# Performance work log

Hardware: AMD Instinct MI355X
Metric: run time of the kernel (lower is better)

Reference implementation:

```python
import jax, jax.numpy as jnp
import numpy as np


def setup_inputs() -> dict:
    key = jax.random.key(0)
    ks = jax.random.split(key, 6)
    Bsz, Ch, N, L = 16, 1024, 16, 4096
    return {
        "input": jax.random.normal(ks[0], (Bsz, Ch, L), jnp.float32),
        "A": jax.random.normal(ks[1], (Ch, N, 2), jnp.float32),
        "B": jax.random.normal(ks[2], (Ch, N), jnp.float32),  # unused in 'dws' mode
        "C": jax.random.normal(ks[3], (Ch, N), jnp.float32),  # unused in 'dws' mode
        "log_dt": jax.random.normal(ks[4], (Ch, N), jnp.float32) * 0.5 - 4.0,
        "E": jax.random.normal(ks[5], (Ch, N), jnp.float32),
    }


def reference(input, A, B, C, log_dt, E):
    """Kernelizer forward, mode='dws', run_mode='training'.

    discretize (simplified ZOH):
      A_real = -softplus(A[...,0]); A_imag = A[...,1]; dt = exp(log_dt)
      E_hat = E * dt; dtA = dt * (A_real + i*A_imag)        # (Ch, N)
    kernel: k[c, l] = Re( sum_n E_hat[c,n] * exp(dtA[c,n] * l) )
    output: causal depthwise conv of input with k via 2L-padded FFT.
    """
    L = input.shape[-1]
    A_real = -jax.nn.softplus(A[..., 0])                     # (Ch, N)
    A_imag = A[..., 1]                                       # (Ch, N)
    dt = jnp.exp(log_dt)                                     # (Ch, N)
    E_hat = E * dt                                           # (Ch, N)
    dtA_real = dt * A_real
    dtA_imag = dt * A_imag

    l = jnp.arange(L, dtype=input.dtype)                     # (L,)
    # real part of the complex vandermonde, fused: exp(ar*l) * cos(ai*l)
    vand = jnp.exp(dtA_real[:, :, None] * l) * jnp.cos(dtA_imag[:, :, None] * l)  # (Ch, N, L)
    k = jnp.einsum('cn,cnl->cl', E_hat, vand)                # (Ch, L)

    n_fft = 2 * L  # zero-pad so circular conv == linear causal conv
    Uf = jnp.fft.rfft(input, n=n_fft)                        # (B, Ch, L+1)
    Kf = jnp.fft.rfft(k, n=n_fft)                            # (Ch, L+1)
    y = jnp.fft.irfft(Uf * Kf, n=n_fft)[..., :L]             # (B, Ch, L)
    return y.astype(input.dtype)
```

## Files before the change

### kernel.cpp

```cpp
#include <hip/hip_runtime.h>
#include <hip/hip_bf16.h>

#define CH   1024
#define BSZ  16
#define LSEQ 4096
#define NST  16

typedef __attribute__((ext_vector_type(8))) short short8;
typedef __attribute__((ext_vector_type(4))) float f32x4;

__device__ __forceinline__ unsigned int pk2(float a, float b) {
    unsigned int ua = __float_as_uint(a);
    unsigned int ub = __float_as_uint(b);
    ua = (ua + 0x7fffu + ((ua >> 16) & 1u)) >> 16;
    ub = (ub + 0x7fffu + ((ub >> 16) & 1u)) & 0xffff0000u;
    return ua | ub;
}
__device__ __forceinline__ unsigned int pkrn(float a, float b) {
    __hip_bfloat162 h = __float22bfloat162_rn(make_float2(a, b));
    unsigned int u;
    __builtin_memcpy(&u, &h, 4);
    return u;
}
__device__ __forceinline__ float rfl(float x) {
    return __int_as_float(__builtin_amdgcn_readfirstlane(__float_as_int(x)));
}
#define DSHR(x, d) __int_as_float(__builtin_amdgcn_update_dpp(0, __float_as_int(x), 0x110 + (d), 0xf, 0xf, true))
#define DBC(x, ctrl, rm) __int_as_float(__builtin_amdgcn_update_dpp(0, __float_as_int(x), (ctrl), (rm), 0xf, true))

#define P_BYTES 12582912
#define W_BYTES 4194304

__global__ __launch_bounds__(64) void setup_k(const float* __restrict__ A,
                                              const float* __restrict__ log_dt,
                                              const float* __restrict__ E,
                                              unsigned int* __restrict__ Pw,
                                              unsigned int* __restrict__ Ww,
                                              float* __restrict__ qw) {
    __shared__ float powr[NST][65], powi[NST][65], eh[NST], klds[64];
    const int t = threadIdx.x, c = blockIdx.x;
    const int n = t & 15;
    const int idx = c * NST + n;
    float a0 = A[2 * idx], a1 = A[2 * idx + 1];
    float sp = (a0 > 20.f) ? a0 : log1pf(expf(a0));
    float dt = expf(log_dt[idx]);
    float dar = -dt * sp, dai = dt * a1;
    float ehv = E[idx] * dt;
    if (t < NST) eh[t] = ehv;
    for (int l = t >> 4; l < 65; l += 4) {
        float mg = expf(dar * (float)l);
        float s, cs;
        sincosf(dai * (float)l, &s, &cs);
        powr[n][l] = mg * cs;
        powi[n][l] = mg * s;
    }
    __syncthreads();
    float kl = 0.f;
#pragma unroll
    for (int nn = 0; nn < NST; ++nn) kl += eh[nn] * powr[nn][t];
    klds[t] = kl;
    __syncthreads();
    unsigned int* Pc = Pw + c * 3072;
    for (int kk = 0; kk < 48; ++kk) {
        int d = kk * 64 + t;
        int i = d / 48;
        int k0 = (d - i * 48) * 2;
        float vv[2];
#pragma unroll
        for (int u = 0; u < 2; ++u) {
            int k = k0 + u;
            if (k < 64) vv[u] = (k <= i) ? klds[i - k] : 0.f;
            else {
                int p = k - 64;
                int nn = p >> 1;
                vv[u] = (p & 1) ? (-eh[nn] * powi[nn][i + 1]) : (eh[nn] * powr[nn][i + 1]);
            }
        }
        Pc[d] = pk2(vv[0], vv[1]);
    }
    unsigned int* Wc = Ww + c * 1024;
    for (int kk = 0; kk < 16; ++kk) {
        int d = kk * 64 + t;
        int p = d >> 5;
        int j0 = (d & 31) * 2;
        int nn = p >> 1;
        float v0 = (p & 1) ? powi[nn][63 - j0] : powr[nn][63 - j0];
        float v1 = (p & 1) ? powi[nn][62 - j0] : powr[nn][62 - j0];
        Wc[d] = pk2(v0, v1);
    }
    if (t < 32) qw[c * 32 + t] = (t & 1) ? powi[t >> 1][64] : powr[t >> 1][64];
}

#define XT0_OFF 0
#define XT1_OFF 8192
#define S_OFF   16384
#define SIN_OFF 24704
#define SMEM_SZ 28800

__global__ __launch_bounds__(256, 4) void conv_k(const float* __restrict__ x,
                                                 const char* __restrict__ Pb,
                                                 const char* __restrict__ Wb,
                                                 const float* __restrict__ qw,
                                                 float* __restrict__ y) {
    __shared__ __align__(16) char smem[SMEM_SZ];
    const int tid  = threadIdx.x;
    const int w    = tid >> 6, lane = tid & 63;
    const int g    = lane >> 4, l15 = lane & 15;
    const int c    = blockIdx.x;

    const char* Pc = Pb + (size_t)c * 12288;
    const char* Wc = Wb + (size_t)c * 4096;
    short8 wa[2], pa[3];
    {
        int p = 16 * (w >> 1) + l15;
#pragma unroll
        for (int kt = 0; kt < 2; ++kt)
            wa[kt] = *(const short8*)(Wc + p * 128 + kt * 64 + g * 16);
        int i = 16 * w + l15;
#pragma unroll
        for (int kt = 0; kt < 3; ++kt)
            pa[kt] = *(const short8*)(Pc + i * 192 + kt * 64 + g * 16);
    }

    float q1r[4], q1i[4], q2r[4], q2i[4], q4r[4], q4i[4], q8r[4], q8i[4];
    float fr[4], fi[4], hr[4], hi[4];
#pragma unroll
    for (int k = 0; k < 4; ++k) {
        int nn = 4 * w + k;
        float ar = qw[c * 32 + 2 * nn], ai = qw[c * 32 + 2 * nn + 1];
        float b2r = fmaf(ar, ar, -(ai * ai)), b2i = 2.f * ar * ai;
        float b4r = fmaf(b2r, b2r, -(b2i * b2i)), b4i = 2.f * b2r * b2i;
        float b8r = fmaf(b4r, b4r, -(b4i * b4i)), b8i = 2.f * b4r * b4i;
        float b16r = fmaf(b8r, b8r, -(b8i * b8i)), b16i = 2.f * b8r * b8i;
        q1r[k] = rfl(ar);  q1i[k] = rfl(ai);
        q2r[k] = rfl(b2r); q2i[k] = rfl(b2i);
        q4r[k] = rfl(b4r); q4i[k] = rfl(b4i);
        q8r[k] = rfl(b8r); q8i[k] = rfl(b8i);
        float cr = ar, ci = ai;
        {
            float tr = fmaf(cr, ar, -(ci * ai)), ti = fmaf(cr, ai, ci * ar);
            cr = (l15 & 1) ? tr : cr; ci = (l15 & 1) ? ti : ci;
        }
        {
            float tr = fmaf(cr, b2r, -(ci * b2i)), ti = fmaf(cr, b2i, ci * b2r);
            cr = (l15 & 2) ? tr : cr; ci = (l15 & 2) ? ti : ci;
        }
        {
            float tr = fmaf(cr, b4r, -(ci * b4i)), ti = fmaf(cr, b4i, ci * b4r);
            cr = (l15 & 4) ? tr : cr; ci = (l15 & 4) ? ti : ci;
        }
        {
            float tr = fmaf(cr, b8r, -(ci * b8i)), ti = fmaf(cr, b8i, ci * b8r);
            cr = (l15 & 8) ? tr : cr; ci = (l15 & 8) ? ti : ci;
        }
        fr[k] = cr; fi[k] = ci;
        float tr = fmaf(cr, b16r, -(ci * b16i)), ti = fmaf(cr, b16i, ci * b16r);
        bool r3 = (lane >= 48);
        hr[k] = r3 ? tr : cr; hi[k] = r3 ? ti : ci;
    }

    int xfo[4][2], sino[4], stb[2];
#pragma unroll
    for (int nt = 0; nt < 4; ++nt) {
#pragma unroll
        for (int kt = 0; kt < 2; ++kt)
            xfo[nt][kt] = ((l15 * 128 + kt * 64 + g * 16) ^ ((l15 & 7) << 4)) + nt * 2048;
        sino[nt] = ((l15 * 64 + g * 16) ^ ((l15 & 3) << 4)) + nt * 1024;
    }
#pragma unroll
    for (int it = 0; it < 2; ++it) {
        int slot = it * 256 + tid;
        int m = slot >> 3, js = slot & 7;
        stb[it] = (m * 128 + js * 16) ^ ((m & 7) << 4);
    }
    const int ntb  = (w & 1) << 1;
    const int swb  = ((16 * (w >> 1) + 4 * g) * 65 + l15 + 16 * ntb) * 4;
    const int srb  = (8 * w * 65 + lane) * 4;
    const int sinw = (lane * 64 + 16 * w) ^ ((lane & 3) << 4);

    float* Sf = (float*)(smem + S_OFF);
    (void)Sf;

    short8 xf[4][2];
    auto rdfrags = [&](int xoff) {
#pragma unroll
        for (int nt = 0; nt < 4; ++nt)
#pragma unroll
            for (int kt = 0; kt < 2; ++kt)
                xf[nt][kt] = *(const short8*)(smem + xoff + xfo[nt][kt]);
    };

    auto gemm1 = [&]() {
        f32x4 a0 = {0.f, 0.f, 0.f, 0.f}, a1 = {0.f, 0.f, 0.f, 0.f};
        if ((w & 1) == 0) {
#pragma unroll
            for (int kt = 0; kt < 2; ++kt) {
                a0 = __builtin_amdgcn_mfma_f32_16x16x32_bf16(wa[kt], xf[0][kt], a0, 0, 0, 0);
                a1 = __builtin_amdgcn_mfma_f32_16x16x32_bf16(wa[kt], xf[1][kt], a1, 0, 0, 0);
            }
        } else {
#pragma unroll
            for (int kt = 0; kt < 2; ++kt) {
                a0 = __builtin_amdgcn_mfma_f32_16x16x32_bf16(wa[kt], xf[2][kt], a0, 0, 0, 0);
                a1 = __builtin_amdgcn_mfma_f32_16x16x32_bf16(wa[kt], xf[3][kt], a1, 0, 0, 0);
            }
        }
#pragma unroll
        for (int r = 0; r < 4; ++r) {
            *(float*)(smem + S_OFF + swb + r * 260)      = a0[r];
            *(float*)(smem + S_OFF + swb + r * 260 + 64) = a1[r];
        }
    };

    auto scan = [&]() {
        float sr[4], si[4];
#pragma unroll
        for (int k = 0; k < 4; ++k) {
            sr[k] = *(const float*)(smem + S_OFF + srb + k * 520);
            si[k] = *(const float*)(smem + S_OFF + srb + k * 520 + 260);
        }
#pragma unroll
        for (int k = 0; k < 4; ++k) {
            { float ur = DSHR(sr[k], 1), ui = DSHR(si[k], 1);
              sr[k] = fmaf(q1r[k], ur, fmaf(-q1i[k], ui, sr[k]));
              si[k] = fmaf(q1r[k], ui, fmaf(q1i[k], ur, si[k])); }
            { float ur = DSHR(sr[k], 2), ui = DSHR(si[k], 2);
              sr[k] = fmaf(q2r[k], ur, fmaf(-q2i[k], ui, sr[k]));
              si[k] = fmaf(q2r[k], ui, fmaf(q2i[k], ur, si[k])); }
            { float ur = DSHR(sr[k], 4), ui = DSHR(si[k], 4);
              sr[k] = fmaf(q4r[k], ur, fmaf(-q4i[k], ui, sr[k]));
              si[k] = fmaf(q4r[k], ui, fmaf(q4i[k], ur, si[k])); }
            { float ur = DSHR(sr[k], 8), ui = DSHR(si[k], 8);
              sr[k] = fmaf(q8r[k], ur, fmaf(-q8i[k], ui, sr[k]));
              si[k] = fmaf(q8r[k], ui, fmaf(q8i[k], ur, si[k])); }
            { float ur = DBC(sr[k], 0x142, 0xa), ui = DBC(si[k], 0x142, 0xa);
              sr[k] = fmaf(fr[k], ur, fmaf(-fi[k], ui, sr[k]));
              si[k] = fmaf(fr[k], ui, fmaf(fi[k], ur, si[k])); }
            { float ur = DBC(sr[k], 0x143, 0xc), ui = DBC(si[k], 0x143, 0xc);
              sr[k] = fmaf(hr[k], ur, fmaf(-hi[k], ui, sr[k]));
              si[k] = fmaf(hr[k], ui, fmaf(hi[k], ur, si[k])); }
        }
        unsigned int dw[4];
#pragma unroll
        for (int k = 0; k < 4; ++k) {
            float ar = __shfl_up(sr[k], 1);
            float ai = __shfl_up(si[k], 1);
            ar = (lane > 0) ? ar : 0.f;
            ai = (lane > 0) ? ai : 0.f;
            dw[k] = pkrn(ar, ai);
        }
        *(uint4*)(smem + SIN_OFF + sinw) = make_uint4(dw[0], dw[1], dw[2], dw[3]);
    };

    auto gemm2 = [&](float* yr) {
        f32x4 acc[4] = {{0.f,0.f,0.f,0.f},{0.f,0.f,0.f,0.f},{0.f,0.f,0.f,0.f},{0.f,0.f,0.f,0.f}};
#pragma unroll
        for (int nt = 0; nt < 4; ++nt) {
            acc[nt] = __builtin_amdgcn_mfma_f32_16x16x32_bf16(pa[0], xf[nt][0], acc[nt], 0, 0, 0);
            short8 sf = *(const short8*)(smem + SIN_OFF + sino[nt]);
            acc[nt] = __builtin_amdgcn_mfma_f32_16x16x32_bf16(pa[2], sf, acc[nt], 0, 0, 0);
        }
        if (w >= 2) {
#pragma unroll
            for (int nt = 0; nt < 4; ++nt)
                acc[nt] = __builtin_amdgcn_mfma_f32_16x16x32_bf16(pa[1], xf[nt][1], acc[nt], 0, 0, 0);
        }
#pragma unroll
        for (int nt = 0; nt < 4; ++nt) {
            int m = l15 + 16 * nt;
            float4 v = make_float4(acc[nt][0], acc[nt][1], acc[nt][2], acc[nt][3]);
            *(float4*)(yr + m * 64 + 16 * w + 4 * g) = v;
        }
    };

    float4 pend[4];
    const float* xr = x + (size_t)c * LSEQ;
    float*       yb = y + (size_t)c * LSEQ;
    const size_t cstride = (size_t)CH * LSEQ;

    auto ldraw = [&](const float* xp) {
#pragma unroll
        for (int it = 0; it < 2; ++it) {
            int slot = it * 256 + tid;
            pend[2 * it]     = *(const float4*)(xp + slot * 8);
            pend[2 * it + 1] = *(const float4*)(xp + slot * 8 + 4);
        }
    };
    auto stage = [&](int xoff) {
#pragma unroll
        for (int it = 0; it < 2; ++it) {
            uint4 pk;
            pk.x = pkrn(pend[2 * it].x,     pend[2 * it].y);
            pk.y = pkrn(pend[2 * it].z,     pend[2 * it].w);
            pk.z = pkrn(pend[2 * it + 1].x, pend[2 * it + 1].y);
            pk.w = pkrn(pend[2 * it + 1].z, pend[2 * it + 1].w);
            *(uint4*)(smem + xoff + stb[it]) = pk;
        }
    };

    ldraw(xr);
    stage(XT0_OFF);
    ldraw(xr + cstride);
    __syncthreads();

#pragma unroll 1
    for (int bb = 0; bb < 8; ++bb) {
        rdfrags(XT0_OFF);
        gemm1();
        __syncthreads();
        scan();
        stage(XT1_OFF);
        if (bb < 7) ldraw(xr + (size_t)(2 * bb + 2) * cstride);
        __syncthreads();
        gemm2(yb + (size_t)(2 * bb) * cstride);

        rdfrags(XT1_OFF);
        gemm1();
        __syncthreads();
        scan();
        if (bb < 7) {
            stage(XT0_OFF);
            ldraw(xr + (size_t)(2 * bb + 3) * cstride);
        }
        __syncthreads();
        gemm2(yb + (size_t)(2 * bb + 1) * cstride);
    }
}

extern "C" void kernel_launch(void* const* d_in, const int* in_sizes, int n_in,
                              void* d_out, int out_size, void* d_ws, size_t ws_size,
                              hipStream_t stream) {
    const float* x      = (const float*)d_in[0];
    const float* A      = (const float*)d_in[1];
    const float* log_dt = (const float*)d_in[4];
    const float* E      = (const float*)d_in[5];
    float* out = (float*)d_out;
    char*  ws  = (char*)d_ws;

    unsigned int* Pw = (unsigned int*)ws;
    unsigned int* Ww = (unsigned int*)(ws + P_BYTES);
    float*        qw = (float*)(ws + P_BYTES + W_BYTES);

    setup_k<<<CH, 64, 0, stream>>>(A, log_dt, E, Pw, Ww, qw);
    conv_k<<<CH, 256, 0, stream>>>(x, (const char*)Pw, (const char*)Ww, qw, out);
}
```

Baseline: 127.1 us.

## Fuse kernel setup into conv kernel and split batch across two blocks

Removes the separate setup kernel: each conv block now computes the per-channel SSM powers, kernel taps and bf16 MFMA operand fragments in shared memory itself, so the workspace round-trip and the second launch go away. The grid doubles to two blocks per channel, each handling half the batch, which raises parallelism but makes both blocks of a channel repeat the setup work. Barriers are replaced by a lighter s_waitcnt lgkmcnt(0) plus s_barrier, which no longer waits for outstanding global loads.

```diff
diff --git a/kernel.cpp b/kernel.cpp
--- a/kernel.cpp
+++ b/kernel.cpp
@@ -9,13 +9,6 @@
 typedef __attribute__((ext_vector_type(8))) short short8;
 typedef __attribute__((ext_vector_type(4))) float f32x4;
 
-__device__ __forceinline__ unsigned int pk2(float a, float b) {
-    unsigned int ua = __float_as_uint(a);
-    unsigned int ub = __float_as_uint(b);
-    ua = (ua + 0x7fffu + ((ua >> 16) & 1u)) >> 16;
-    ub = (ub + 0x7fffu + ((ub >> 16) & 1u)) & 0xffff0000u;
-    return ua | ub;
-}
 __device__ __forceinline__ unsigned int pkrn(float a, float b) {
     __hip_bfloat162 h = __float22bfloat162_rn(make_float2(a, b));
     unsigned int u;
@@ -28,98 +21,130 @@
 #define DSHR(x, d) __int_as_float(__builtin_amdgcn_update_dpp(0, __float_as_int(x), 0x110 + (d), 0xf, 0xf, true))
 #define DBC(x, ctrl, rm) __int_as_float(__builtin_amdgcn_update_dpp(0, __float_as_int(x), (ctrl), (rm), 0xf, true))
 
-#define P_BYTES 12582912
-#define W_BYTES 4194304
-
-__global__ __launch_bounds__(64) void setup_k(const float* __restrict__ A,
-                                              const float* __restrict__ log_dt,
-                                              const float* __restrict__ E,
-                                              unsigned int* __restrict__ Pw,
-                                              unsigned int* __restrict__ Ww,
-                                              float* __restrict__ qw) {
-    __shared__ float powr[NST][65], powi[NST][65], eh[NST], klds[64];
-    const int t = threadIdx.x, c = blockIdx.x;
-    const int n = t & 15;
-    const int idx = c * NST + n;
-    float a0 = A[2 * idx], a1 = A[2 * idx + 1];
-    float sp = (a0 > 20.f) ? a0 : log1pf(expf(a0));
-    float dt = expf(log_dt[idx]);
-    float dar = -dt * sp, dai = dt * a1;
-    float ehv = E[idx] * dt;
-    if (t < NST) eh[t] = ehv;
-    for (int l = t >> 4; l < 65; l += 4) {
-        float mg = expf(dar * (float)l);
-        float s, cs;
-        sincosf(dai * (float)l, &s, &cs);
-        powr[n][l] = mg * cs;
-        powi[n][l] = mg * s;
-    }
-    __syncthreads();
-    float kl = 0.f;
-#pragma unroll
-    for (int nn = 0; nn < NST; ++nn) kl += eh[nn] * powr[nn][t];
-    klds[t] = kl;
-    __syncthreads();
-    unsigned int* Pc = Pw + c * 3072;
-    for (int kk = 0; kk < 48; ++kk) {
-        int d = kk * 64 + t;
-        int i = d / 48;
-        int k0 = (d - i * 48) * 2;
-        float vv[2];
-#pragma unroll
-        for (int u = 0; u < 2; ++u) {
-            int k = k0 + u;
-            if (k < 64) vv[u] = (k <= i) ? klds[i - k] : 0.f;
-            else {
-                int p = k - 64;
-                int nn = p >> 1;
-                vv[u] = (p & 1) ? (-eh[nn] * powi[nn][i + 1]) : (eh[nn] * powr[nn][i + 1]);
-            }
-        }
-        Pc[d] = pk2(vv[0], vv[1]);
-    }
-    unsigned int* Wc = Ww + c * 1024;
-    for (int kk = 0; kk < 16; ++kk) {
-        int d = kk * 64 + t;
-        int p = d >> 5;
-        int j0 = (d & 31) * 2;
-        int nn = p >> 1;
-        float v0 = (p & 1) ? powi[nn][63 - j0] : powr[nn][63 - j0];
-        float v1 = (p & 1) ? powi[nn][62 - j0] : powr[nn][62 - j0];
-        Wc[d] = pk2(v0, v1);
-    }
-    if (t < 32) qw[c * 32 + t] = (t & 1) ? powi[t >> 1][64] : powr[t >> 1][64];
-}
-
 #define XT0_OFF 0
 #define XT1_OFF 8192
 #define S_OFF   16384
 #define SIN_OFF 24704
 #define SMEM_SZ 28800
 
+__device__ __forceinline__ void barrier_fast() {
+    asm volatile("s_waitcnt lgkmcnt(0)\n\ts_barrier" ::: "memory");
+}
+
 __global__ __launch_bounds__(256, 4) void conv_k(const float* __restrict__ x,
-                                                 const char* __restrict__ Pb,
-                                                 const char* __restrict__ Wb,
-                                                 const float* __restrict__ qw,
+                                                 const float* __restrict__ A,
+                                                 const float* __restrict__ log_dt,
+                                                 const float* __restrict__ E,
                                                  float* __restrict__ y) {
     __shared__ __align__(16) char smem[SMEM_SZ];
     const int tid  = threadIdx.x;
     const int w    = tid >> 6, lane = tid & 63;
     const int g    = lane >> 4, l15 = lane & 15;
-    const int c    = blockIdx.x;
-
-    const char* Pc = Pb + (size_t)c * 12288;
-    const char* Wc = Wb + (size_t)c * 4096;
+    const int bid  = blockIdx.x;
+    const int c    = bid >> 1;
+    const int half = bid & 1;
+
+    const size_t cstride = (size_t)CH * LSEQ;
+    const float* xr = x + ((size_t)(8 * half) * CH + c) * (size_t)LSEQ;
+    float*       yb = y + ((size_t)(8 * half) * CH + c) * (size_t)LSEQ;
+
+    int stb[2];
+#pragma unroll
+    for (int it = 0; it < 2; ++it) {
+        int slot = it * 256 + tid;
+        int m = slot >> 3, js = slot & 7;
+        stb[it] = (m * 128 + js * 16) ^ ((m & 7) << 4);
+    }
+    float4 pend[4];
+    auto ldraw = [&](const float* xp) {
+#pragma unroll
+        for (int it = 0; it < 2; ++it) {
+            int slot = it * 256 + tid;
+            pend[2 * it]     = *(const float4*)(xp + slot * 8);
+            pend[2 * it + 1] = *(const float4*)(xp + slot * 8 + 4);
+        }
+    };
+    auto stage = [&](int xoff) {
+#pragma unroll
+        for (int it = 0; it < 2; ++it) {
+            uint4 pk;
+            pk.x = pkrn(pend[2 * it].x,     pend[2 * it].y);
+            pk.y = pkrn(pend[2 * it].z,     pend[2 * it].w);
+            pk.z = pkrn(pend[2 * it + 1].x, pend[2 * it + 1].y);
+            pk.w = pkrn(pend[2 * it + 1].z, pend[2 * it + 1].w);
+            *(uint4*)(smem + xoff + stb[it]) = pk;
+        }
+    };
+
+    ldraw(xr);
+
+    float* PR = (float*)(smem + S_OFF);
+    float* PI = PR + NST * 65;
+    float* EH = (float*)(smem + SIN_OFF);
+    float* KL = EH + NST;
+    {
+        int n = tid & 15;
+        int idx0 = c * NST + n;
+        float a0 = A[2 * idx0], a1 = A[2 * idx0 + 1];
+        float sp = (a0 > 20.f) ? a0 : log1pf(expf(a0));
+        float dtv = expf(log_dt[idx0]);
+        float dar = -dtv * sp, dai = dtv * a1;
+        if (tid < NST) EH[tid] = E[idx0] * dtv;
+        for (int l = tid >> 4; l < 65; l += 16) {
+            float mg = expf(dar * (float)l);
+            float s, cs;
+            sincosf(dai * (float)l, &s, &cs);
+            PR[n * 65 + l] = mg * cs;
+            PI[n * 65 + l] = mg * s;
+        }
+    }
+    __syncthreads();
+    if (tid < 64) {
+        float kl = 0.f;
+#pragma unroll
+        for (int nn = 0; nn < NST; ++nn) kl += EH[nn] * PR[nn * 65 + tid];
+        KL[tid] = kl;
+    }
+    __syncthreads();
+
     short8 wa[2], pa[3];
     {
         int p = 16 * (w >> 1) + l15;
-#pragma unroll
-        for (int kt = 0; kt < 2; ++kt)
-            wa[kt] = *(const short8*)(Wc + p * 128 + kt * 64 + g * 16);
+        const float* tb = ((p & 1) ? PI : PR) + (p >> 1) * 65;
+#pragma unroll
+        for (int kt = 0; kt < 2; ++kt) {
+            union { short8 v; unsigned int d[4]; } u;
+#pragma unroll
+            for (int e2 = 0; e2 < 4; ++e2) {
+                int j = kt * 32 + 8 * g + 2 * e2;
+                u.d[e2] = pkrn(tb[63 - j], tb[62 - j]);
+            }
+            wa[kt] = u.v;
+        }
         int i = 16 * w + l15;
 #pragma unroll
-        for (int kt = 0; kt < 3; ++kt)
-            pa[kt] = *(const short8*)(Pc + i * 192 + kt * 64 + g * 16);
+        for (int kt = 0; kt < 2; ++kt) {
+            union { short8 v; unsigned int d[4]; } u;
+#pragma unroll
+            for (int e2 = 0; e2 < 4; ++e2) {
+                int k0 = kt * 32 + 8 * g + 2 * e2;
+                float v0 = (k0 <= i)     ? KL[i - k0]     : 0.f;
+                float v1 = (k0 + 1 <= i) ? KL[i - k0 - 1] : 0.f;
+                u.d[e2] = pkrn(v0, v1);
+            }
+            pa[kt] = u.v;
+        }
+        {
+            union { short8 v; unsigned int d[4]; } u;
+#pragma unroll
+            for (int e2 = 0; e2 < 4; ++e2) {
+                int n3 = 4 * g + e2;
+                float re = EH[n3] * PR[n3 * 65 + i + 1];
+                float im = -EH[n3] * PI[n3 * 65 + i + 1];
+                u.d[e2] = pkrn(re, im);
+            }
+            pa[2] = u.v;
+        }
     }
 
     float q1r[4], q1i[4], q2r[4], q2i[4], q4r[4], q4i[4], q8r[4], q8i[4];
@@ -127,7 +152,7 @@
 #pragma unroll
     for (int k = 0; k < 4; ++k) {
         int nn = 4 * w + k;
-        float ar = qw[c * 32 + 2 * nn], ai = qw[c * 32 + 2 * nn + 1];
+        float ar = PR[nn * 65 + 64], ai = PI[nn * 65 + 64];
         float b2r = fmaf(ar, ar, -(ai * ai)), b2i = 2.f * ar * ai;
         float b4r = fmaf(b2r, b2r, -(b2i * b2i)), b4i = 2.f * b2r * b2i;
         float b8r = fmaf(b4r, b4r, -(b4i * b4i)), b8i = 2.f * b4r * b4i;
@@ -159,27 +184,18 @@
         hr[k] = r3 ? tr : cr; hi[k] = r3 ? ti : ci;
     }
 
-    int xfo[4][2], sino[4], stb[2];
+    int xfo[4][2], sino[4];
 #pragma unroll
     for (int nt = 0; nt < 4; ++nt) {
 #pragma unroll
         for (int kt = 0; kt < 2; ++kt)
             xfo[nt][kt] = ((l15 * 128 + kt * 64 + g * 16) ^ ((l15 & 7) << 4)) + nt * 2048;
         sino[nt] = ((l15 * 64 + g * 16) ^ ((l15 & 3) << 4)) + nt * 1024;
-    }
-#pragma unroll
-    for (int it = 0; it < 2; ++it) {
-        int slot = it * 256 + tid;
-        int m = slot >> 3, js = slot & 7;
-        stb[it] = (m * 128 + js * 16) ^ ((m & 7) << 4);
     }
     const int ntb  = (w & 1) << 1;
     const int swb  = ((16 * (w >> 1) + 4 * g) * 65 + l15 + 16 * ntb) * 4;
     const int srb  = (8 * w * 65 + lane) * 4;
     const int sinw = (lane * 64 + 16 * w) ^ ((lane & 3) << 4);
-
-    float* Sf = (float*)(smem + S_OFF);
-    (void)Sf;
 
     short8 xf[4][2];
     auto rdfrags = [&](int xoff) {
@@ -273,56 +289,30 @@
         }
     };
 
-    float4 pend[4];
-    const float* xr = x + (size_t)c * LSEQ;
-    float*       yb = y + (size_t)c * LSEQ;
-    const size_t cstride = (size_t)CH * LSEQ;
-
-    auto ldraw = [&](const float* xp) {
-#pragma unroll
-        for (int it = 0; it < 2; ++it) {
-            int slot = it * 256 + tid;
-            pend[2 * it]     = *(const float4*)(xp + slot * 8);
-            pend[2 * it + 1] = *(const float4*)(xp + slot * 8 + 4);
-        }
-    };
-    auto stage = [&](int xoff) {
-#pragma unroll
-        for (int it = 0; it < 2; ++it) {
-            uint4 pk;
-            pk.x = pkrn(pend[2 * it].x,     pend[2 * it].y);
-            pk.y = pkrn(pend[2 * it].z,     pend[2 * it].w);
-            pk.z = pkrn(pend[2 * it + 1].x, pend[2 * it + 1].y);
-            pk.w = pkrn(pend[2 * it + 1].z, pend[2 * it + 1].w);
-            *(uint4*)(smem + xoff + stb[it]) = pk;
-        }
-    };
-
-    ldraw(xr);
     stage(XT0_OFF);
     ldraw(xr + cstride);
     __syncthreads();
 
 #pragma unroll 1
-    for (int bb = 0; bb < 8; ++bb) {
+    for (int bb = 0; bb < 4; ++bb) {
         rdfrags(XT0_OFF);
         gemm1();
-        __syncthreads();
+        barrier_fast();
         scan();
         stage(XT1_OFF);
-        if (bb < 7) ldraw(xr + (size_t)(2 * bb + 2) * cstride);
-        __syncthreads();
+        if (bb < 3) ldraw(xr + (size_t)(2 * bb + 2) * cstride);
+        barrier_fast();
         gemm2(yb + (size_t)(2 * bb) * cstride);
 
         rdfrags(XT1_OFF);
         gemm1();
-        __syncthreads();
+        barrier_fast();
         scan();
-        if (bb < 7) {
+        if (bb < 3) {
             stage(XT0_OFF);
             ldraw(xr + (size_t)(2 * bb + 3) * cstride);
         }
-        __syncthreads();
+        barrier_fast();
         gemm2(yb + (size_t)(2 * bb + 1) * cstride);
     }
 }
@@ -335,12 +325,7 @@
     const float* log_dt = (const float*)d_in[4];
     const float* E      = (const float*)d_in[5];
     float* out = (float*)d_out;
-    char*  ws  = (char*)d_ws;
-
-    unsigned int* Pw = (unsigned int*)ws;
-    unsigned int* Ww = (unsigned int*)(ws + P_BYTES);
-    float*        qw = (float*)(ws + P_BYTES + W_BYTES);
-
-    setup_k<<<CH, 64, 0, stream>>>(A, log_dt, E, Pw, Ww, qw);
-    conv_k<<<CH, 256, 0, stream>>>(x, (const char*)Pw, (const char*)Ww, qw, out);
-}
+    (void)d_ws; (void)ws_size;
+
+    conv_k<<<2 * CH, 256, 0, stream>>>(x, A, log_dt, E, out);
+}
```

After: 110.7 us. -12.9%, faster.
